# Kernel tuning notes

Measured on AMD Instinct MI355X. Metric: run time of the kernel, lower is better.

The kernel has to match this reference:

```python
import jax, jax.numpy as jnp
import numpy as np

H = 1024  # hidden_size
B, S = 64, 2048


def setup_inputs() -> dict:
    key = jax.random.key(0)
    ks = jax.random.split(key, 9)
    d = {
        "s_t": jax.random.normal(ks[0], (B, 2 * H), jnp.float32),
        "h_i": jax.random.normal(ks[1], (B, S, 2 * H), jnp.float32),
        "coverage": jax.random.uniform(ks[2], (B, S), jnp.float32),
        # parameters (torch Linear: y = x @ W.T + b)
        "W_h": jax.random.normal(ks[3], (H, 2 * H), jnp.float32) / np.sqrt(2 * H),
        "b_h": jnp.zeros((H,), jnp.float32),
        "W_s": jax.random.normal(ks[4], (H, 2 * H), jnp.float32) / np.sqrt(2 * H),
        "b_s": jnp.zeros((H,), jnp.float32),
        "W_c": jax.random.normal(ks[5], (H, 1), jnp.float32),  # no bias
        "v_a": jax.random.normal(ks[6], (1, H), jnp.float32) / np.sqrt(H),
        "b_a": jnp.zeros((1,), jnp.float32),
    }
    return d


def reference(s_t, h_i, coverage, W_h, b_h, W_s, b_s, W_c, v_a, b_a):
    # Wi_hi: (B,S,H)
    Wi_hi = jnp.einsum("bsd,hd->bsh", h_i, W_h) + b_h
    # Ws_s: (B,H)
    Ws_s = jnp.einsum("bd,hd->bh", s_t, W_s) + b_s
    # coverage features: (B,S,H)  (W_c is (H,1))
    cov_feat = coverage[:, :, None] * W_c[:, 0]
    # scores: (B,S)
    E = jnp.einsum("bsh,h->bs", jnp.tanh(Wi_hi + Ws_s[:, None, :] + cov_feat), v_a[0]) + b_a[0]
    A = jax.nn.softmax(E, axis=-1)
    # context: (B,2H)
    C = jnp.einsum("bs,bsd->bd", A, h_i)
    new_cov = coverage + A
    return (C, A, new_cov)
```

## Files before the change

### kernel.cpp

```cpp
#include <hip/hip_runtime.h>
#include <hip/hip_bf16.h>

typedef __bf16 bf16x8_v __attribute__((ext_vector_type(8)));
typedef float  f32x4_v  __attribute__((ext_vector_type(4)));

static constexpr int kH = 1024;
static constexpr int kD = 2048;
static constexpr int kB = 64;
static constexpr int kS = 2048;
static constexpr int kM = kB * kS;

__device__ __forceinline__ void load_lds16(const void* g, void* l) {
  __builtin_amdgcn_global_load_lds(
      (const __attribute__((address_space(1))) unsigned int*)g,
      (__attribute__((address_space(3))) unsigned int*)l, 16, 0, 0);
}

__device__ __forceinline__ float fast_tanh(float x) {
  float e = __expf(2.0f * x);
  return 1.0f - 2.0f * __builtin_amdgcn_rcpf(e + 1.0f);
}

__global__ __launch_bounds__(256) void conv_tile_kernel(const float* __restrict__ in,
                                                        __bf16* __restrict__ out) {
  size_t g = (size_t)blockIdx.x * 256 + threadIdx.x;
  int p = (int)(g & 63);
  size_t tile = g >> 6;
  int kt = (int)(tile & 63);
  size_t mt16 = tile >> 6;
  int rr = p >> 2, s = p & 3;
  int c = s ^ ((rr >> 1) & 3);
  const float* src = in + (mt16 * 16 + rr) * (size_t)kD + kt * 32 + c * 8;
  float4 v0 = reinterpret_cast<const float4*>(src)[0];
  float4 v1 = reinterpret_cast<const float4*>(src)[1];
  bf16x8_v o = {(__bf16)v0.x, (__bf16)v0.y, (__bf16)v0.z, (__bf16)v0.w,
                (__bf16)v1.x, (__bf16)v1.y, (__bf16)v1.z, (__bf16)v1.w};
  reinterpret_cast<bf16x8_v*>(out)[g] = o;
}

__global__ __launch_bounds__(256) void prep_bias_kernel(
    const float* __restrict__ s_t, const float* __restrict__ W_s,
    const float* __restrict__ b_s, const float* __restrict__ b_h,
    float* __restrict__ biasBH) {
  int wave = blockIdx.x * 4 + (threadIdx.x >> 6);
  int lane = threadIdx.x & 63;
  int b = wave >> 10, h = wave & 1023;
  const float4* sp = reinterpret_cast<const float4*>(s_t + (size_t)b * kD);
  const float4* wp = reinterpret_cast<const float4*>(W_s + (size_t)h * kD);
  float acc = 0.f;
  for (int i = lane; i < kD / 4; i += 64) {
    float4 a = sp[i], w = wp[i];
    acc += a.x * w.x + a.y * w.y + a.z * w.z + a.w * w.w;
  }
  for (int m = 1; m < 64; m <<= 1) acc += __shfl_xor(acc, m);
  if (lane == 0) biasBH[wave] = acc + b_s[h] + b_h[h];
}

__global__ __launch_bounds__(512, 2) void gemm_score_kernel(
    const float* __restrict__ h_i,
    const __bf16* __restrict__ Wtl,
    const float* __restrict__ biasBH,
    const float* __restrict__ coverage,
    const float* __restrict__ Wc,
    const float* __restrict__ va,
    float* __restrict__ E) {
  const int bid = blockIdx.x;
  const int xcd = bid & 7;
  const int slot = bid >> 3;
  const int n0 = (slot & 3) * 256;
  const int m0 = (xcd * 64 + (slot >> 2)) * 256;

  const int tid = threadIdx.x;
  const int lane = tid & 63;
  const int wid = tid >> 6;
  const int wm = wid >> 2, wn = wid & 3;

  __shared__ char lds[3 * 49152];

  f32x4_v acc[8][4];
#pragma unroll
  for (int m = 0; m < 8; ++m)
#pragma unroll
    for (int n = 0; n < 4; ++n) acc[m][n] = {0.f, 0.f, 0.f, 0.f};

  const int l15 = lane & 15;
  const int j = lane >> 4;
  const int s7 = lane & 7;
  const int aco0 = ((2 * j) ^ s7) << 4;
  const int aco1 = aco0 ^ 16;
  const int slot16 = ((j ^ ((l15 >> 1) & 3)) << 4);

  const int awr = lane >> 3;
  const int awc = (lane & 7) ^ awr;
  const float* Asrc[4];
  char* Adst[4];
#pragma unroll
  for (int w = 0; w < 4; ++w) {
    int win = wid * 4 + w;
    Asrc[w] = h_i + (size_t)(m0 + win * 8 + awr) * kD + awc * 4;
    Adst[w] = (char*)lds + win * 1024;
  }
  const int nt16b = (slot & 3) * 16;
  const __bf16* Bsrc[2];
  char* Bdst[2];
#pragma unroll
  for (int s = 0; s < 2; ++s) {
    Bsrc[s] = Wtl + ((size_t)(nt16b + wid * 2 + s) * 64) * 512 + lane * 8;
    Bdst[s] = (char*)lds + 32768 + (wid * 2 + s) * 1024;
  }

#define STAGE(T)                                                       \
  do {                                                                 \
    int bo = ((T) % 3) * 49152;                                        \
    load_lds16(Asrc[0] + (T) * 32, Adst[0] + bo);                      \
    load_lds16(Asrc[1] + (T) * 32, Adst[1] + bo);                      \
    load_lds16(Asrc[2] + (T) * 32, Adst[2] + bo);                      \
    load_lds16(Asrc[3] + (T) * 32, Adst[3] + bo);                      \
    load_lds16(Bsrc[0] + (size_t)(T) * 512, Bdst[0] + bo);             \
    load_lds16(Bsrc[1] + (size_t)(T) * 512, Bdst[1] + bo);             \
  } while (0)

#define RD_A(AF, I, AB)                                                          \
  do {                                                                           \
    int row = wm * 128 + (I) * 16 + l15;                                         \
    const char* base = (AB) + row * 128;                                         \
    f32x4_v lo = *reinterpret_cast<const f32x4_v*>(base + aco0);                 \
    f32x4_v hi = *reinterpret_cast<const f32x4_v*>(base + aco1);                 \
    AF = bf16x8_v{(__bf16)lo[0], (__bf16)lo[1], (__bf16)lo[2], (__bf16)lo[3],    \
                  (__bf16)hi[0], (__bf16)hi[1], (__bf16)hi[2], (__bf16)hi[3]};   \
  } while (0)

#define TILE(T, DO_STAGE, WAITN)                                       \
  do {                                                                 \
    asm volatile("s_waitcnt vmcnt(" #WAITN ")" ::: "memory");          \
    __builtin_amdgcn_s_barrier();                                      \
    asm volatile("" ::: "memory");                                     \
    if (DO_STAGE) STAGE((T) + 2);                                      \
    const char* Ab = (const char*)lds + ((T) % 3) * 49152;             \
    const char* Bb = Ab + 32768;                                       \
    bf16x8_v b[4];                                                     \
    _Pragma("unroll")                                                  \
    for (int n = 0; n < 4; ++n) {                                      \
      int row = wn * 64 + n * 16 + l15;                                \
      b[n] = *reinterpret_cast<const bf16x8_v*>(                       \
          Bb + (row >> 4) * 1024 + (row & 15) * 64 + slot16);          \
    }                                                                  \
    bf16x8_v a0, a1, a2, a3;                                           \
    RD_A(a0, 0, Ab); RD_A(a1, 1, Ab); RD_A(a2, 2, Ab); RD_A(a3, 3, Ab);\
    __builtin_amdgcn_s_setprio(1);                                     \
    _Pragma("unroll")                                                  \
    for (int n = 0; n < 4; ++n) {                                      \
      acc[0][n] = __builtin_amdgcn_mfma_f32_16x16x32_bf16(a0, b[n], acc[0][n], 0, 0, 0); \
      acc[1][n] = __builtin_amdgcn_mfma_f32_16x16x32_bf16(a1, b[n], acc[1][n], 0, 0, 0); \
      acc[2][n] = __builtin_amdgcn_mfma_f32_16x16x32_bf16(a2, b[n], acc[2][n], 0, 0, 0); \
      acc[3][n] = __builtin_amdgcn_mfma_f32_16x16x32_bf16(a3, b[n], acc[3][n], 0, 0, 0); \
    }                                                                  \
    __builtin_amdgcn_s_setprio(0);                                     \
    RD_A(a0, 4, Ab); RD_A(a1, 5, Ab); RD_A(a2, 6, Ab); RD_A(a3, 7, Ab);\
    __builtin_amdgcn_s_setprio(1);                                     \
    _Pragma("unroll")                                                  \
    for (int n = 0; n < 4; ++n) {                                      \
      acc[4][n] = __builtin_amdgcn_mfma_f32_16x16x32_bf16(a0, b[n], acc[4][n], 0, 0, 0); \
      acc[5][n] = __builtin_amdgcn_mfma_f32_16x16x32_bf16(a1, b[n], acc[5][n], 0, 0, 0); \
      acc[6][n] = __builtin_amdgcn_mfma_f32_16x16x32_bf16(a2, b[n], acc[6][n], 0, 0, 0); \
      acc[7][n] = __builtin_amdgcn_mfma_f32_16x16x32_bf16(a3, b[n], acc[7][n], 0, 0, 0); \
    }                                                                  \
    __builtin_amdgcn_s_setprio(0);                                     \
  } while (0)

  STAGE(0);
  STAGE(1);

  for (int t = 0; t < 60; t += 3) {
    TILE(t, 1, 6);
    TILE(t + 1, 1, 6);
    TILE(t + 2, 1, 6);
  }
  TILE(60, 1, 6);
  TILE(61, 1, 6);
  TILE(62, 0, 6);
  TILE(63, 0, 0);

#undef STAGE
#undef RD_A
#undef TILE

  const int bb = m0 >> 11;
  const int colg = lane & 15;
  const int rowg = lane >> 4;
  float bias_v[4], wc_v[4], va_v[4];
#pragma unroll
  for (int n = 0; n < 4; ++n) {
    int h = n0 + wn * 64 + n * 16 + colg;
    bias_v[n] = biasBH[bb * kH + h];
    wc_v[n] = Wc[h];
    va_v[n] = va[h];
  }
  const int s_tile = (m0 & (kS - 1));
#pragma unroll
  for (int m = 0; m < 8; ++m) {
    int sbase = s_tile + wm * 128 + m * 16 + rowg * 4;
    float cov[4], rowsum[4];
#pragma unroll
    for (int q = 0; q < 4; ++q) {
      cov[q] = coverage[bb * kS + sbase + q];
      rowsum[q] = 0.f;
    }
#pragma unroll
    for (int n = 0; n < 4; ++n) {
#pragma unroll
      for (int q = 0; q < 4; ++q) {
        float z = acc[m][n][q] + bias_v[n] + cov[q] * wc_v[n];
        rowsum[q] += fast_tanh(z) * va_v[n];
      }
    }
#pragma unroll
    for (int q = 0; q < 4; ++q) {
      float v = rowsum[q];
      v += __shfl_xor(v, 1);
      v += __shfl_xor(v, 2);
      v += __shfl_xor(v, 4);
      v += __shfl_xor(v, 8);
      if (colg == 0) atomicAdd(&E[bb * kS + sbase + q], v);
    }
  }
}

__global__ __launch_bounds__(256) void softmax_kernel(
    const float* __restrict__ E, const float* __restrict__ coverage,
    float* __restrict__ A, float* __restrict__ newcov) {
  int b = blockIdx.x;
  int tid = threadIdx.x;
  int wid = tid >> 6, lane = tid & 63;
  __shared__ float wred[4];
  float ev[8];
  float mx = -INFINITY;
#pragma unroll
  for (int i = 0; i < 8; ++i) {
    ev[i] = E[b * kS + tid + i * 256];
    mx = fmaxf(mx, ev[i]);
  }
  for (int m = 1; m < 64; m <<= 1) mx = fmaxf(mx, __shfl_xor(mx, m));
  if (lane == 0) wred[wid] = mx;
  __syncthreads();
  mx = fmaxf(fmaxf(wred[0], wred[1]), fmaxf(wred[2], wred[3]));
  __syncthreads();
  float sum = 0.f;
#pragma unroll
  for (int i = 0; i < 8; ++i) {
    ev[i] = __expf(ev[i] - mx);
    sum += ev[i];
  }
  for (int m = 1; m < 64; m <<= 1) sum += __shfl_xor(sum, m);
  if (lane == 0) wred[wid] = sum;
  __syncthreads();
  sum = wred[0] + wred[1] + wred[2] + wred[3];
  float inv = 1.f / sum;
#pragma unroll
  for (int i = 0; i < 8; ++i) {
    int s = tid + i * 256;
    float a = ev[i] * inv;
    A[b * kS + s] = a;
    newcov[b * kS + s] = coverage[b * kS + s] + a;
  }
}

__global__ __launch_bounds__(256) void context_kernel(
    const float* __restrict__ h_i, const float* __restrict__ A,
    float* __restrict__ C) {
  int b = blockIdx.x;
  int d = blockIdx.y * 1024 + threadIdx.x * 4;
  int s0 = blockIdx.z * 256;
  const float* hp = h_i + ((size_t)b * kS + s0) * kD + d;
  const float* ap = A + b * kS + s0;
  float4 acc = {0.f, 0.f, 0.f, 0.f};
  for (int s = 0; s < 256; ++s) {
    float a = ap[s];
    float4 v = *reinterpret_cast<const float4*>(hp + (size_t)s * kD);
    acc.x += a * v.x;
    acc.y += a * v.y;
    acc.z += a * v.z;
    acc.w += a * v.w;
  }
  atomicAdd(&C[b * kD + d + 0], acc.x);
  atomicAdd(&C[b * kD + d + 1], acc.y);
  atomicAdd(&C[b * kD + d + 2], acc.z);
  atomicAdd(&C[b * kD + d + 3], acc.w);
}

extern "C" void kernel_launch(void* const* d_in, const int* in_sizes, int n_in,
                              void* d_out, int out_size, void* d_ws, size_t ws_size,
                              hipStream_t stream) {
  const float* s_t      = (const float*)d_in[0];
  const float* h_i      = (const float*)d_in[1];
  const float* coverage = (const float*)d_in[2];
  const float* W_h      = (const float*)d_in[3];
  const float* b_h      = (const float*)d_in[4];
  const float* W_s      = (const float*)d_in[5];
  const float* b_s      = (const float*)d_in[6];
  const float* W_c      = (const float*)d_in[7];
  const float* v_a      = (const float*)d_in[8];

  float* out = (float*)d_out;
  float* C      = out;
  float* A      = out + kB * kD;
  float* newcov = A + kB * kS;

  char* ws = (char*)d_ws;
  __bf16* Wtl   = (__bf16*)ws;
  float* biasBH = (float*)(ws + (4u << 20));
  float* E      = (float*)(ws + (4u << 20) + (256u << 10));

  hipMemsetAsync(E, 0, (size_t)kB * kS * sizeof(float), stream);
  hipMemsetAsync(C, 0, (size_t)kB * kD * sizeof(float), stream);

  conv_tile_kernel<<<kH, 256, 0, stream>>>(W_h, Wtl);
  prep_bias_kernel<<<(kB * kH) / 4, 256, 0, stream>>>(s_t, W_s, b_s, b_h, biasBH);

  gemm_score_kernel<<<2048, 512, 0, stream>>>(h_i, Wtl, biasBH, coverage,
                                              W_c, v_a, E);

  softmax_kernel<<<kB, 256, 0, stream>>>(E, coverage, A, newcov);

  dim3 gc(kB, kD / 1024, kS / 256);
  context_kernel<<<gc, 256, 0, stream>>>(h_i, A, C);
}
```

Measured before the change: 851.2 us.

## Convert A tile to bf16 in registers before LDS, double-buffer staging

The fp32 activation tile used to be copied straight into LDS through async global-to-LDS loads, then converted to bf16 on every LDS read. Now each thread loads the fp32 values into registers, converts them to bf16 once, and writes a swizzled bf16 tile to LDS. This halves the A footprint in LDS and cuts LDS read traffic and repeated conversions. The triple buffer becomes a double buffer with a software-pipelined register prefetch. The trade-offs are more VGPR pressure, an extra barrier per K step, and a shallower async pipeline for the weight tiles.

Result: slower. 943.9 us (+10.9%).

```diff
diff --git a/kernel.cpp b/kernel.cpp
--- a/kernel.cpp
+++ b/kernel.cpp
@@ -67,7 +67,8 @@
   const int bid = blockIdx.x;
   const int xcd = bid & 7;
   const int slot = bid >> 3;
-  const int n0 = (slot & 3) * 256;
+  const int nblk = slot & 3;
+  const int n0 = nblk * 256;
   const int m0 = (xcd * 64 + (slot >> 2)) * 256;
 
   const int tid = threadIdx.x;
@@ -75,7 +76,7 @@
   const int wid = tid >> 6;
   const int wm = wid >> 2, wn = wid & 3;
 
-  __shared__ char lds[3 * 49152];
+  __shared__ char lds[2 * 32768];
 
   f32x4_v acc[8][4];
 #pragma unroll
@@ -85,105 +86,120 @@
 
   const int l15 = lane & 15;
   const int j = lane >> 4;
-  const int s7 = lane & 7;
-  const int aco0 = ((2 * j) ^ s7) << 4;
-  const int aco1 = aco0 ^ 16;
-  const int slot16 = ((j ^ ((l15 >> 1) & 3)) << 4);
-
-  const int awr = lane >> 3;
-  const int awc = (lane & 7) ^ awr;
-  const float* Asrc[4];
-  char* Adst[4];
-#pragma unroll
-  for (int w = 0; w < 4; ++w) {
-    int win = wid * 4 + w;
-    Asrc[w] = h_i + (size_t)(m0 + win * 8 + awr) * kD + awc * 4;
-    Adst[w] = (char*)lds + win * 1024;
-  }
-  const int nt16b = (slot & 3) * 16;
-  const __bf16* Bsrc[2];
-  char* Bdst[2];
-#pragma unroll
-  for (int s = 0; s < 2; ++s) {
-    Bsrc[s] = Wtl + ((size_t)(nt16b + wid * 2 + s) * 64) * 512 + lane * 8;
-    Bdst[s] = (char*)lds + 32768 + (wid * 2 + s) * 1024;
-  }
-
-#define STAGE(T)                                                       \
-  do {                                                                 \
-    int bo = ((T) % 3) * 49152;                                        \
-    load_lds16(Asrc[0] + (T) * 32, Adst[0] + bo);                      \
-    load_lds16(Asrc[1] + (T) * 32, Adst[1] + bo);                      \
-    load_lds16(Asrc[2] + (T) * 32, Adst[2] + bo);                      \
-    load_lds16(Asrc[3] + (T) * 32, Adst[3] + bo);                      \
-    load_lds16(Bsrc[0] + (size_t)(T) * 512, Bdst[0] + bo);             \
-    load_lds16(Bsrc[1] + (size_t)(T) * 512, Bdst[1] + bo);             \
-  } while (0)
-
-#define RD_A(AF, I, AB)                                                          \
-  do {                                                                           \
-    int row = wm * 128 + (I) * 16 + l15;                                         \
-    const char* base = (AB) + row * 128;                                         \
-    f32x4_v lo = *reinterpret_cast<const f32x4_v*>(base + aco0);                 \
-    f32x4_v hi = *reinterpret_cast<const f32x4_v*>(base + aco1);                 \
-    AF = bf16x8_v{(__bf16)lo[0], (__bf16)lo[1], (__bf16)lo[2], (__bf16)lo[3],    \
-                  (__bf16)hi[0], (__bf16)hi[1], (__bf16)hi[2], (__bf16)hi[3]};   \
-  } while (0)
-
-#define TILE(T, DO_STAGE, WAITN)                                       \
-  do {                                                                 \
-    asm volatile("s_waitcnt vmcnt(" #WAITN ")" ::: "memory");          \
-    __builtin_amdgcn_s_barrier();                                      \
-    asm volatile("" ::: "memory");                                     \
-    if (DO_STAGE) STAGE((T) + 2);                                      \
-    const char* Ab = (const char*)lds + ((T) % 3) * 49152;             \
-    const char* Bb = Ab + 32768;                                       \
-    bf16x8_v b[4];                                                     \
-    _Pragma("unroll")                                                  \
-    for (int n = 0; n < 4; ++n) {                                      \
-      int row = wn * 64 + n * 16 + l15;                                \
-      b[n] = *reinterpret_cast<const bf16x8_v*>(                       \
-          Bb + (row >> 4) * 1024 + (row & 15) * 64 + slot16);          \
-    }                                                                  \
-    bf16x8_v a0, a1, a2, a3;                                           \
-    RD_A(a0, 0, Ab); RD_A(a1, 1, Ab); RD_A(a2, 2, Ab); RD_A(a3, 3, Ab);\
-    __builtin_amdgcn_s_setprio(1);                                     \
-    _Pragma("unroll")                                                  \
-    for (int n = 0; n < 4; ++n) {                                      \
-      acc[0][n] = __builtin_amdgcn_mfma_f32_16x16x32_bf16(a0, b[n], acc[0][n], 0, 0, 0); \
-      acc[1][n] = __builtin_amdgcn_mfma_f32_16x16x32_bf16(a1, b[n], acc[1][n], 0, 0, 0); \
-      acc[2][n] = __builtin_amdgcn_mfma_f32_16x16x32_bf16(a2, b[n], acc[2][n], 0, 0, 0); \
-      acc[3][n] = __builtin_amdgcn_mfma_f32_16x16x32_bf16(a3, b[n], acc[3][n], 0, 0, 0); \
-    }                                                                  \
-    __builtin_amdgcn_s_setprio(0);                                     \
-    RD_A(a0, 4, Ab); RD_A(a1, 5, Ab); RD_A(a2, 6, Ab); RD_A(a3, 7, Ab);\
-    __builtin_amdgcn_s_setprio(1);                                     \
-    _Pragma("unroll")                                                  \
-    for (int n = 0; n < 4; ++n) {                                      \
-      acc[4][n] = __builtin_amdgcn_mfma_f32_16x16x32_bf16(a0, b[n], acc[4][n], 0, 0, 0); \
-      acc[5][n] = __builtin_amdgcn_mfma_f32_16x16x32_bf16(a1, b[n], acc[5][n], 0, 0, 0); \
-      acc[6][n] = __builtin_amdgcn_mfma_f32_16x16x32_bf16(a2, b[n], acc[6][n], 0, 0, 0); \
-      acc[7][n] = __builtin_amdgcn_mfma_f32_16x16x32_bf16(a3, b[n], acc[7][n], 0, 0, 0); \
-    }                                                                  \
-    __builtin_amdgcn_s_setprio(0);                                     \
-  } while (0)
-
-  STAGE(0);
-  STAGE(1);
-
-  for (int t = 0; t < 60; t += 3) {
-    TILE(t, 1, 6);
-    TILE(t + 1, 1, 6);
-    TILE(t + 2, 1, 6);
-  }
-  TILE(60, 1, 6);
-  TILE(61, 1, 6);
-  TILE(62, 0, 6);
-  TILE(63, 0, 0);
-
-#undef STAGE
-#undef RD_A
+  const int slot16 = (j ^ ((l15 >> 1) & 3)) << 4;
+
+  const int arow = wid * 32 + (lane >> 1);
+  const int ah = lane & 1;
+  const float* Ag = h_i + (size_t)(m0 + arow) * kD + ah * 16;
+  const int ast = arow >> 4;
+  const int arr = arow & 15;
+  const int ax = (arr >> 1) & 3;
+  const int aw0 = ast * 1024 + arr * 64 + (((2 * ah) ^ ax) << 4);
+  const int aw1 = ast * 1024 + arr * 64 + (((2 * ah + 1) ^ ax) << 4);
+
+  const __bf16* Bsrc0 = Wtl + ((size_t)(nblk * 16 + wid * 2) * 64) * 512 + lane * 8;
+  const __bf16* Bsrc1 = Wtl + ((size_t)(nblk * 16 + wid * 2 + 1) * 64) * 512 + lane * 8;
+
+  f32x4_v avP[4], avQ[4];
+
+#define LOADA(T, AV)                                                  \
+  do {                                                                \
+    const float* p_ = Ag + (size_t)(T) * 32;                          \
+    AV[0] = *reinterpret_cast<const f32x4_v*>(p_);                    \
+    AV[1] = *reinterpret_cast<const f32x4_v*>(p_ + 4);                \
+    AV[2] = *reinterpret_cast<const f32x4_v*>(p_ + 8);                \
+    AV[3] = *reinterpret_cast<const f32x4_v*>(p_ + 12);               \
+  } while (0)
+
+#define WRITEA(AV, B)                                                 \
+  do {                                                                \
+    char* base_ = lds + (B) * 32768;                                  \
+    bf16x8_v o0_ = {(__bf16)AV[0][0], (__bf16)AV[0][1], (__bf16)AV[0][2], (__bf16)AV[0][3], \
+                    (__bf16)AV[1][0], (__bf16)AV[1][1], (__bf16)AV[1][2], (__bf16)AV[1][3]}; \
+    bf16x8_v o1_ = {(__bf16)AV[2][0], (__bf16)AV[2][1], (__bf16)AV[2][2], (__bf16)AV[2][3], \
+                    (__bf16)AV[3][0], (__bf16)AV[3][1], (__bf16)AV[3][2], (__bf16)AV[3][3]}; \
+    *reinterpret_cast<bf16x8_v*>(base_ + aw0) = o0_;                  \
+    *reinterpret_cast<bf16x8_v*>(base_ + aw1) = o1_;                  \
+  } while (0)
+
+#define GLOADB(T, B)                                                  \
+  do {                                                                \
+    load_lds16(Bsrc0 + (size_t)(T) * 512, lds + (B) * 32768 + 16384 + (wid * 2) * 1024); \
+    load_lds16(Bsrc1 + (size_t)(T) * 512, lds + (B) * 32768 + 16384 + (wid * 2 + 1) * 1024); \
+  } while (0)
+
+#define TILE(T, WAITN)                                                \
+  do {                                                                \
+    asm volatile("s_waitcnt vmcnt(" #WAITN ")" ::: "memory");         \
+    __builtin_amdgcn_s_barrier();                                     \
+    __builtin_amdgcn_sched_barrier(0);                                \
+    const char* Ab_ = lds + ((T) & 1) * 32768;                        \
+    const char* Bb_ = Ab_ + 16384;                                    \
+    bf16x8_v b_[4], a_[4];                                            \
+    _Pragma("unroll")                                                 \
+    for (int n = 0; n < 4; ++n)                                       \
+      b_[n] = *reinterpret_cast<const bf16x8_v*>(                     \
+          Bb_ + (wn * 4 + n) * 1024 + l15 * 64 + slot16);             \
+    _Pragma("unroll")                                                 \
+    for (int mi = 0; mi < 4; ++mi)                                    \
+      a_[mi] = *reinterpret_cast<const bf16x8_v*>(                    \
+          Ab_ + (wm * 8 + mi) * 1024 + l15 * 64 + slot16);            \
+    __builtin_amdgcn_s_setprio(1);                                    \
+    _Pragma("unroll")                                                 \
+    for (int mi = 0; mi < 4; ++mi)                                    \
+      _Pragma("unroll")                                               \
+      for (int n = 0; n < 4; ++n)                                     \
+        acc[mi][n] = __builtin_amdgcn_mfma_f32_16x16x32_bf16(a_[mi], b_[n], acc[mi][n], 0, 0, 0); \
+    __builtin_amdgcn_s_setprio(0);                                    \
+    _Pragma("unroll")                                                 \
+    for (int mi = 0; mi < 4; ++mi)                                    \
+      a_[mi] = *reinterpret_cast<const bf16x8_v*>(                    \
+          Ab_ + (wm * 8 + 4 + mi) * 1024 + l15 * 64 + slot16);        \
+    __builtin_amdgcn_s_setprio(1);                                    \
+    _Pragma("unroll")                                                 \
+    for (int mi = 0; mi < 4; ++mi)                                    \
+      _Pragma("unroll")                                               \
+      for (int n = 0; n < 4; ++n)                                     \
+        acc[4 + mi][n] = __builtin_amdgcn_mfma_f32_16x16x32_bf16(a_[mi], b_[n], acc[4 + mi][n], 0, 0, 0); \
+    __builtin_amdgcn_s_setprio(0);                                    \
+  } while (0)
+
+#define POSTE(T, AV)                                                  \
+  do {                                                                \
+    WRITEA(AV, ((T) + 1) & 1);                   \
+    asm volatile("s_waitcnt lgkmcnt(0)" ::: "memory");                \
+    __builtin_amdgcn_s_barrier();                                     \
+    __builtin_amdgcn_sched_barrier(0);                                \
+    if ((T) + 2 < 64) GLOADB((T) + 2, (T) & 1);                       \
+    if ((T) + 3 < 64) LOADA((T) + 3, AV);                             \
+  } while (0)
+
+  LOADA(0, avP);
+  asm volatile("s_waitcnt vmcnt(0)" ::: "memory");
+  WRITEA(avP, 0);
+  GLOADB(0, 0);
+  LOADA(1, avP);
+  GLOADB(1, 1);
+  LOADA(2, avQ);
+  asm volatile("s_waitcnt lgkmcnt(0)" ::: "memory");
+  __builtin_amdgcn_s_barrier();
+  __builtin_amdgcn_sched_barrier(0);
+
+  for (int t = 0; t < 62; t += 2) {
+    TILE(t, 6);
+    POSTE(t, avP);
+    TILE(t + 1, 6);
+    POSTE(t + 1, avQ);
+  }
+  TILE(62, 2);
+  POSTE(62, avP);
+  TILE(63, 0);
+
+#undef LOADA
+#undef WRITEA
+#undef GLOADB
 #undef TILE
+#undef POSTE
 
   const int bb = m0 >> 11;
   const int colg = lane & 15;
```
